# Kernel optimization log

Measured on AMD Instinct MI355X. Metric: run time of the kernel, lower is better.

Reference implementation:

```python
import jax, jax.numpy as jnp
import numpy as np

D_MODEL = 1024
N_HEAD = 16
HEAD_DIM = D_MODEL // N_HEAD
B, S = 4, 2048


def setup_inputs() -> dict:
    key = jax.random.key(0)
    ks = jax.random.split(key, 11)
    s = 1.0 / np.sqrt(D_MODEL)
    return {
        "query": jax.random.normal(ks[0], (B, S, D_MODEL), jnp.float32),
        "key": jax.random.normal(ks[1], (B, S, D_MODEL), jnp.float32),
        "value": jax.random.normal(ks[2], (B, S, D_MODEL), jnp.float32),
        "Wq": jax.random.normal(ks[3], (D_MODEL, D_MODEL), jnp.float32) * s,
        "bq": jax.random.normal(ks[4], (D_MODEL,), jnp.float32) * s,
        "Wk": jax.random.normal(ks[5], (D_MODEL, D_MODEL), jnp.float32) * s,
        "bk": jax.random.normal(ks[6], (D_MODEL,), jnp.float32) * s,
        "Wv": jax.random.normal(ks[7], (D_MODEL, D_MODEL), jnp.float32) * s,
        "bv": jax.random.normal(ks[8], (D_MODEL,), jnp.float32) * s,
        "Wo": jax.random.normal(ks[9], (D_MODEL, D_MODEL), jnp.float32) * s,
        "bo": jax.random.normal(ks[10], (D_MODEL,), jnp.float32) * s,
    }


def reference(query, key, value, Wq, bq, Wk, bk, Wv, bv, Wo, bo):
    b, s, d_model = query.shape
    # projections; reshape to [b, h, s, hd]
    def proj(x, W, bias):
        return (x @ W + bias).reshape(b, s, N_HEAD, HEAD_DIM).transpose(0, 2, 1, 3)
    q = proj(query, Wq, bq)
    k = proj(key, Wk, bk)
    v = proj(value, Wv, bv)
    # NOTE: original code scales by sqrt(d_model) (bug-faithful), not sqrt(head_dim)
    scores = jnp.einsum("bhqd,bhkd->bhqk", q, k) / jnp.sqrt(jnp.float32(d_model))
    causal = jnp.tril(jnp.ones((s, s), dtype=bool))
    scores = jnp.where(causal[None, None], scores, -jnp.inf)
    p = jax.nn.softmax(scores, axis=-1)  # dropout is identity in eval
    x = jnp.einsum("bhqk,bhkd->bhqd", p, v)
    x = x.transpose(0, 2, 1, 3).reshape(b, s, d_model)
    return x @ Wo + bo
```

## Files before the change

### kernel.cpp

```cpp
#include <hip/hip_runtime.h>
#include <hip/hip_bf16.h>
#include <cstdint>
#include <cstddef>

#define D_MODEL 1024
#define N_HEAD 16
#define HEAD_DIM 64
#define BATCH 4
#define SEQ 2048
#define M_ROWS (BATCH * SEQ)

typedef __attribute__((ext_vector_type(8))) short short8v;
typedef __attribute__((ext_vector_type(4))) float f32x4;
typedef __attribute__((ext_vector_type(16))) float f32x16;

__device__ __forceinline__ unsigned short f2bf(float f) {
    union { uint32_t i; float f; } c;
    c.f = f;
    uint32_t r = c.i + 0x7FFFu + ((c.i >> 16) & 1u);
    return (unsigned short)(r >> 16);
}
__device__ __forceinline__ unsigned short trunc_bf(float f) {
    return (unsigned short)(__float_as_uint(f) >> 16);
}
__device__ __forceinline__ uint32_t pack_trunc2(float a, float b) {
    return __builtin_amdgcn_perm(__float_as_uint(b), __float_as_uint(a), 0x07060302u);
}

struct __align__(16) U4 { uint32_t x, y, z, w; };
struct __align__(8) U2 { uint32_t x, y; };

__device__ __forceinline__ int sw_off(int row, int gl) {
    return row * 64 + ((gl ^ (row & 7)) << 3);
}

__global__ __launch_bounds__(256)
void wtrans_kernel(const float *__restrict__ W, unsigned short *__restrict__ Wt)
{
    __shared__ float tile[32][33];
    const int t = threadIdx.x;
    const int tx = t & 31, ty = t >> 5;
    const int bk = blockIdx.y * 32, bn = blockIdx.x * 32;
#pragma unroll
    for (int i = 0; i < 4; i++)
        tile[ty + 8 * i][tx] = W[(size_t)(bk + ty + 8 * i) * D_MODEL + bn + tx];
    __syncthreads();
#pragma unroll
    for (int i = 0; i < 4; i++)
        Wt[(size_t)(bn + ty + 8 * i) * D_MODEL + bk + tx] = trunc_bf(tile[tx][ty + 8 * i]);
}

template <typename TA, int MODE, typename TO>
__global__ __launch_bounds__(256, 2)
void mgemm_kernel(const TA *__restrict__ A,
                  const unsigned short *__restrict__ Wt,
                  const float *__restrict__ bias,
                  TO *__restrict__ out,
                  float escale)
{
    __shared__ __align__(16) unsigned short At[128 * 64];
    __shared__ __align__(16) unsigned short Bt[128 * 64];

    const int t = threadIdx.x;
    const int wave = t >> 6;
    const int lane = t & 63;
    const int n_ = lane & 15;
    const int quad = lane >> 4;
    const int wm = wave >> 1, wn = wave & 1;
    const int m0 = blockIdx.x * 128;
    const int n0 = blockIdx.y * 128;

    f32x4 acc[4][4];
#pragma unroll
    for (int i = 0; i < 4; i++)
#pragma unroll
        for (int j = 0; j < 4; j++) acc[i][j] = (f32x4){0.f, 0.f, 0.f, 0.f};

    const int srow = t >> 3;
    const int sg = t & 7;

    for (int k0 = 0; k0 < D_MODEL; k0 += 64) {
        __syncthreads();
#pragma unroll
        for (int i = 0; i < 4; i++) {
            const int r = srow + 32 * i;
            if constexpr (sizeof(TA) == 4) {
                const float *p = (const float *)A + (size_t)(m0 + r) * D_MODEL + k0 + sg * 8;
                float4 lo = *(const float4 *)p;
                float4 hi = *(const float4 *)(p + 4);
                U4 pk;
                pk.x = pack_trunc2(lo.x, lo.y);
                pk.y = pack_trunc2(lo.z, lo.w);
                pk.z = pack_trunc2(hi.x, hi.y);
                pk.w = pack_trunc2(hi.z, hi.w);
                *(U4 *)&At[sw_off(r, sg)] = pk;
            } else {
                const unsigned short *p =
                    (const unsigned short *)A + (size_t)(m0 + r) * D_MODEL + k0 + sg * 8;
                *(U4 *)&At[sw_off(r, sg)] = *(const U4 *)p;
            }
        }
#pragma unroll
        for (int i = 0; i < 4; i++) {
            const int r = srow + 32 * i;
            const unsigned short *p = Wt + (size_t)(n0 + r) * D_MODEL + k0 + sg * 8;
            *(U4 *)&Bt[sw_off(r, sg)] = *(const U4 *)p;
        }
        __syncthreads();

#pragma unroll
        for (int c = 0; c < 2; c++) {
            short8v af[4], bf[4];
#pragma unroll
            for (int mt = 0; mt < 4; mt++)
                af[mt] = *(const short8v *)&At[sw_off(wm * 64 + mt * 16 + n_, c * 4 + quad)];
#pragma unroll
            for (int nt = 0; nt < 4; nt++)
                bf[nt] = *(const short8v *)&Bt[sw_off(wn * 64 + nt * 16 + n_, c * 4 + quad)];
#pragma unroll
            for (int mt = 0; mt < 4; mt++)
#pragma unroll
                for (int nt = 0; nt < 4; nt++)
                    acc[mt][nt] =
                        __builtin_amdgcn_mfma_f32_16x16x32_bf16(af[mt], bf[nt], acc[mt][nt], 0, 0, 0);
        }
    }

    float bi[4];
#pragma unroll
    for (int nt = 0; nt < 4; nt++) bi[nt] = bias[n0 + wn * 64 + nt * 16 + n_];

#pragma unroll
    for (int mt = 0; mt < 4; mt++) {
#pragma unroll
        for (int reg = 0; reg < 4; reg++) {
            const int m = m0 + wm * 64 + mt * 16 + quad * 4 + reg;
#pragma unroll
            for (int nt = 0; nt < 4; nt++) {
                const int col = n0 + wn * 64 + nt * 16 + n_;
                const float v = (acc[mt][nt][reg] + bi[nt]) * escale;
                if constexpr (MODE == 1) {
                    ((unsigned short *)out)[(size_t)m * D_MODEL + col] = f2bf(v);
                } else if constexpr (MODE == 2) {
                    const size_t idx = ((size_t)(m >> 11) * D_MODEL + col) * SEQ + (m & 2047);
                    ((unsigned short *)out)[idx] = f2bf(v);
                } else {
                    ((float *)out)[(size_t)m * D_MODEL + col] = v;
                }
            }
        }
    }
}

__global__ __launch_bounds__(256, 2)
void attn_kernel(const unsigned short *Qg,
                 const unsigned short *__restrict__ Kg,
                 const unsigned short *__restrict__ VTg,
                 unsigned short *AO)
{
    __shared__ __align__(16) unsigned short Kt[64 * 64];
    __shared__ __align__(16) unsigned short Vt[64 * 64];

    const int h = blockIdx.x;
    const int b = blockIdx.y;
    const int qpair = blockIdx.z;
    const int t = threadIdx.x;
    const int w = t >> 6;
    const int lane = t & 63;
    const int ql = lane & 31;
    const int hi = lane >> 5;

    const size_t row_base = (size_t)b * SEQ * D_MODEL + h * HEAD_DIM;
    const size_t vhead = (size_t)(b * N_HEAD + h) * HEAD_DIM * SEQ;

    const int r0 = t >> 3;
    const int g = t & 7;

#pragma unroll
    for (int pass = 0; pass < 2; ++pass) {
        const int qb = pass ? (15 - qpair) : qpair;
        const int qs0 = qb * 128 + w * 32;
        const int qseq = qs0 + ql;

        short8v qf[4];
#pragma unroll
        for (int c = 0; c < 4; c++)
            qf[c] = *(const short8v *)(Qg + row_base + (size_t)qseq * D_MODEL + c * 16 + hi * 8);

        float m_i = -INFINITY, l_i = 0.f;
        f32x16 Oacc[2];
#pragma unroll
        for (int dt = 0; dt < 2; dt++)
#pragma unroll
            for (int i = 0; i < 16; i++) Oacc[dt][i] = 0.f;

        const int kb_max = 2 * qb + 1;

        for (int kb = 0; kb <= kb_max; ++kb) {
            __syncthreads();
#pragma unroll
            for (int i = 0; i < 2; i++) {
                const int r = r0 + 32 * i;
                U4 kv = *(const U4 *)(Kg + row_base + (size_t)(kb * 64 + r) * D_MODEL + g * 8);
                *(U4 *)&Kt[sw_off(r, g)] = kv;
                U4 vv = *(const U4 *)(VTg + vhead + (size_t)r * SEQ + kb * 64 + g * 8);
                *(U4 *)&Vt[sw_off(r, g)] = vv;
            }
            __syncthreads();

            if (kb * 64 > qs0 + 31) continue;

            f32x16 st[2];
            __builtin_amdgcn_s_setprio(1);
#pragma unroll
            for (int kt = 0; kt < 2; kt++) {
#pragma unroll
                for (int i = 0; i < 16; i++) st[kt][i] = 0.f;
#pragma unroll
                for (int c = 0; c < 4; c++) {
                    short8v kf = *(const short8v *)&Kt[sw_off(kt * 32 + ql, c * 2 + hi)];
                    st[kt] = __builtin_amdgcn_mfma_f32_32x32x16_bf16(kf, qf[c], st[kt], 0, 0, 0);
                }
            }
            __builtin_amdgcn_s_setprio(0);

            if (kb * 64 + 63 > qs0) {
#pragma unroll
                for (int kt = 0; kt < 2; kt++)
#pragma unroll
                    for (int r = 0; r < 16; r++) {
                        const int kseq = kb * 64 + kt * 32 + (r & 3) + 8 * (r >> 2) + 4 * hi;
                        if (kseq > qseq) st[kt][r] = -INFINITY;
                    }
            }

            float mx = -INFINITY;
#pragma unroll
            for (int kt = 0; kt < 2; kt++)
#pragma unroll
                for (int r = 0; r < 16; r++) mx = fmaxf(mx, st[kt][r]);
            mx = fmaxf(mx, __shfl_xor(mx, 32, 64));
            const float mnew = fmaxf(m_i, mx);
            const float alpha = __builtin_amdgcn_exp2f(m_i - mnew);
            m_i = mnew;
            float rs = 0.f;
#pragma unroll
            for (int kt = 0; kt < 2; kt++)
#pragma unroll
                for (int r = 0; r < 16; r++) {
                    const float p = __builtin_amdgcn_exp2f(st[kt][r] - mnew);
                    st[kt][r] = p;
                    rs += p;
                }
            rs += __shfl_xor(rs, 32, 64);
            l_i = l_i * alpha + rs;
#pragma unroll
            for (int dt = 0; dt < 2; dt++)
#pragma unroll
                for (int r = 0; r < 16; r++) Oacc[dt][r] *= alpha;

            short8v pf[4];
#pragma unroll
            for (int tt = 0; tt < 4; tt++) {
                const int kt = tt >> 1, o = (tt & 1) * 8;
                const uint32_t A  = pack_trunc2(st[kt][o + 0], st[kt][o + 1]);
                const uint32_t A2 = pack_trunc2(st[kt][o + 2], st[kt][o + 3]);
                const uint32_t B  = pack_trunc2(st[kt][o + 4], st[kt][o + 5]);
                const uint32_t B2 = pack_trunc2(st[kt][o + 6], st[kt][o + 7]);
                const uint32_t c1 = (uint32_t)__shfl_xor((int)(hi ? A : B), 32, 64);
                const uint32_t c2 = (uint32_t)__shfl_xor((int)(hi ? A2 : B2), 32, 64);
                union { uint32_t u[4]; short8v s; } cv;
                cv.u[0] = hi ? c1 : A;
                cv.u[1] = hi ? c2 : A2;
                cv.u[2] = hi ? B : c1;
                cv.u[3] = hi ? B2 : c2;
                pf[tt] = cv.s;
            }

            __builtin_amdgcn_s_setprio(1);
#pragma unroll
            for (int dt = 0; dt < 2; dt++)
#pragma unroll
                for (int tt = 0; tt < 4; tt++) {
                    short8v vf = *(const short8v *)&Vt[sw_off(dt * 32 + ql, tt * 2 + hi)];
                    Oacc[dt] = __builtin_amdgcn_mfma_f32_32x32x16_bf16(vf, pf[tt], Oacc[dt], 0, 0, 0);
                }
            __builtin_amdgcn_s_setprio(0);
        }

        const float linv = 1.f / l_i;
        const size_t obase = row_base + (size_t)qseq * D_MODEL;
#pragma unroll
        for (int dt = 0; dt < 2; dt++)
#pragma unroll
            for (int rg = 0; rg < 4; rg++) {
                const int d0 = dt * 32 + 8 * rg + 4 * hi;
                U2 pk;
                pk.x = (uint32_t)f2bf(Oacc[dt][4 * rg + 0] * linv) |
                       ((uint32_t)f2bf(Oacc[dt][4 * rg + 1] * linv) << 16);
                pk.y = (uint32_t)f2bf(Oacc[dt][4 * rg + 2] * linv) |
                       ((uint32_t)f2bf(Oacc[dt][4 * rg + 3] * linv) << 16);
                *(U2 *)(AO + obase + d0) = pk;
            }
    }
}

extern "C" void kernel_launch(void *const *d_in, const int *in_sizes, int n_in,
                              void *d_out, int out_size, void *d_ws, size_t ws_size,
                              hipStream_t stream)
{
    const float *q  = (const float *)d_in[0];
    const float *k  = (const float *)d_in[1];
    const float *v  = (const float *)d_in[2];
    const float *Wq = (const float *)d_in[3];
    const float *bq = (const float *)d_in[4];
    const float *Wk = (const float *)d_in[5];
    const float *bk = (const float *)d_in[6];
    const float *Wv = (const float *)d_in[7];
    const float *bv = (const float *)d_in[8];
    const float *Wo = (const float *)d_in[9];
    const float *bo = (const float *)d_in[10];
    float *out = (float *)d_out;

    const size_t TENS = (size_t)M_ROWS * D_MODEL;
    unsigned short *qbuf = (unsigned short *)d_ws;
    unsigned short *kbuf = qbuf + TENS;
    unsigned short *vtbuf = kbuf + TENS;
    unsigned short *wt = vtbuf + TENS;

    dim3 wgrid(32, 32);
    dim3 ggrid(M_ROWS / 128, D_MODEL / 128);

    const float qscale = 0.03125f * 1.44269504088896341f;

    wtrans_kernel<<<wgrid, 256, 0, stream>>>(Wq, wt);
    mgemm_kernel<float, 1, unsigned short><<<ggrid, 256, 0, stream>>>(q, wt, bq, qbuf, qscale);
    wtrans_kernel<<<wgrid, 256, 0, stream>>>(Wk, wt);
    mgemm_kernel<float, 1, unsigned short><<<ggrid, 256, 0, stream>>>(k, wt, bk, kbuf, 1.f);
    wtrans_kernel<<<wgrid, 256, 0, stream>>>(Wv, wt);
    mgemm_kernel<float, 2, unsigned short><<<ggrid, 256, 0, stream>>>(v, wt, bv, vtbuf, 1.f);

    attn_kernel<<<dim3(N_HEAD, BATCH, SEQ / 256), 256, 0, stream>>>(qbuf, kbuf, vtbuf, qbuf);

    wtrans_kernel<<<wgrid, 256, 0, stream>>>(Wo, wt);
    mgemm_kernel<unsigned short, 3, float><<<ggrid, 256, 0, stream>>>(qbuf, wt, bo, out, 1.f);
}
```

Baseline: 381.0 us.

## Use direct global-to-LDS loads for bf16 GEMM operands and pre-convert activations

New measurement: 323.0 us. 15.2% less time.

```diff
diff --git a/kernel.cpp b/kernel.cpp
--- a/kernel.cpp
+++ b/kernel.cpp
@@ -32,6 +32,25 @@
 
 __device__ __forceinline__ int sw_off(int row, int gl) {
     return row * 64 + ((gl ^ (row & 7)) << 3);
+}
+
+__device__ __forceinline__ void gload16(const unsigned short *g, unsigned short *l) {
+    __builtin_amdgcn_global_load_lds((const __attribute__((address_space(1))) void *)g,
+                                     (__attribute__((address_space(3))) void *)l, 16, 0, 0);
+}
+
+__global__ __launch_bounds__(256)
+void cvt_kernel(const float *__restrict__ src, unsigned short *__restrict__ dst)
+{
+    const size_t i = ((size_t)blockIdx.x * 256 + threadIdx.x) * 8;
+    float4 lo = *(const float4 *)(src + i);
+    float4 hi = *(const float4 *)(src + i + 4);
+    U4 pk;
+    pk.x = pack_trunc2(lo.x, lo.y);
+    pk.y = pack_trunc2(lo.z, lo.w);
+    pk.z = pack_trunc2(hi.x, hi.y);
+    pk.w = pack_trunc2(hi.z, hi.w);
+    *(U4 *)(dst + i) = pk;
 }
 
 __global__ __launch_bounds__(256)
@@ -78,13 +97,24 @@
 
     const int srow = t >> 3;
     const int sg = t & 7;
+    const int rl = lane >> 3;
+    const int gsw = (lane & 7) ^ rl;
 
     for (int k0 = 0; k0 < D_MODEL; k0 += 64) {
         __syncthreads();
-#pragma unroll
-        for (int i = 0; i < 4; i++) {
-            const int r = srow + 32 * i;
-            if constexpr (sizeof(TA) == 4) {
+        if constexpr (sizeof(TA) == 2) {
+#pragma unroll
+            for (int c = 0; c < 4; c++) {
+                const int rb = wave * 32 + c * 8;
+                gload16((const unsigned short *)A + (size_t)(m0 + rb + rl) * D_MODEL + k0 + (gsw << 3),
+                        &At[rb * 64]);
+                gload16(Wt + (size_t)(n0 + rb + rl) * D_MODEL + k0 + (gsw << 3),
+                        &Bt[rb * 64]);
+            }
+        } else {
+#pragma unroll
+            for (int i = 0; i < 4; i++) {
+                const int r = srow + 32 * i;
                 const float *p = (const float *)A + (size_t)(m0 + r) * D_MODEL + k0 + sg * 8;
                 float4 lo = *(const float4 *)p;
                 float4 hi = *(const float4 *)(p + 4);
@@ -94,17 +124,13 @@
                 pk.z = pack_trunc2(hi.x, hi.y);
                 pk.w = pack_trunc2(hi.z, hi.w);
                 *(U4 *)&At[sw_off(r, sg)] = pk;
-            } else {
-                const unsigned short *p =
-                    (const unsigned short *)A + (size_t)(m0 + r) * D_MODEL + k0 + sg * 8;
-                *(U4 *)&At[sw_off(r, sg)] = *(const U4 *)p;
-            }
-        }
-#pragma unroll
-        for (int i = 0; i < 4; i++) {
-            const int r = srow + 32 * i;
-            const unsigned short *p = Wt + (size_t)(n0 + r) * D_MODEL + k0 + sg * 8;
-            *(U4 *)&Bt[sw_off(r, sg)] = *(const U4 *)p;
+            }
+#pragma unroll
+            for (int i = 0; i < 4; i++) {
+                const int r = srow + 32 * i;
+                const unsigned short *p = Wt + (size_t)(n0 + r) * D_MODEL + k0 + sg * 8;
+                *(U4 *)&Bt[sw_off(r, sg)] = *(const U4 *)p;
+            }
         }
         __syncthreads();
 
@@ -326,22 +352,46 @@
     unsigned short *qbuf = (unsigned short *)d_ws;
     unsigned short *kbuf = qbuf + TENS;
     unsigned short *vtbuf = kbuf + TENS;
-    unsigned short *wt = vtbuf + TENS;
+    unsigned short *cbuf = vtbuf + TENS;
+    unsigned short *wt_new = cbuf + TENS;
+    unsigned short *wt_old = vtbuf + TENS;
 
     dim3 wgrid(32, 32);
     dim3 ggrid(M_ROWS / 128, D_MODEL / 128);
+    const int cgrid = (int)(TENS / 8 / 256);
 
     const float qscale = 0.03125f * 1.44269504088896341f;
 
-    wtrans_kernel<<<wgrid, 256, 0, stream>>>(Wq, wt);
-    mgemm_kernel<float, 1, unsigned short><<<ggrid, 256, 0, stream>>>(q, wt, bq, qbuf, qscale);
-    wtrans_kernel<<<wgrid, 256, 0, stream>>>(Wk, wt);
-    mgemm_kernel<float, 1, unsigned short><<<ggrid, 256, 0, stream>>>(k, wt, bk, kbuf, 1.f);
-    wtrans_kernel<<<wgrid, 256, 0, stream>>>(Wv, wt);
-    mgemm_kernel<float, 2, unsigned short><<<ggrid, 256, 0, stream>>>(v, wt, bv, vtbuf, 1.f);
-
-    attn_kernel<<<dim3(N_HEAD, BATCH, SEQ / 256), 256, 0, stream>>>(qbuf, kbuf, vtbuf, qbuf);
-
-    wtrans_kernel<<<wgrid, 256, 0, stream>>>(Wo, wt);
-    mgemm_kernel<unsigned short, 3, float><<<ggrid, 256, 0, stream>>>(qbuf, wt, bo, out, 1.f);
-}
+    const size_t need_new = (5 * TENS + (size_t)D_MODEL * D_MODEL) * sizeof(unsigned short);
+
+    if (ws_size >= need_new) {
+        unsigned short *wt = wt_new;
+        wtrans_kernel<<<wgrid, 256, 0, stream>>>(Wq, wt);
+        cvt_kernel<<<cgrid, 256, 0, stream>>>(q, cbuf);
+        mgemm_kernel<unsigned short, 1, unsigned short><<<ggrid, 256, 0, stream>>>(cbuf, wt, bq, qbuf, qscale);
+        wtrans_kernel<<<wgrid, 256, 0, stream>>>(Wk, wt);
+        cvt_kernel<<<cgrid, 256, 0, stream>>>(k, cbuf);
+        mgemm_kernel<unsigned short, 1, unsigned short><<<ggrid, 256, 0, stream>>>(cbuf, wt, bk, kbuf, 1.f);
+        wtrans_kernel<<<wgrid, 256, 0, stream>>>(Wv, wt);
+        cvt_kernel<<<cgrid, 256, 0, stream>>>(v, cbuf);
+        mgemm_kernel<unsigned short, 2, unsigned short><<<ggrid, 256, 0, stream>>>(cbuf, wt, bv, vtbuf, 1.f);
+
+        attn_kernel<<<dim3(N_HEAD, BATCH, SEQ / 256), 256, 0, stream>>>(qbuf, kbuf, vtbuf, qbuf);
+
+        wtrans_kernel<<<wgrid, 256, 0, stream>>>(Wo, wt);
+        mgemm_kernel<unsigned short, 3, float><<<ggrid, 256, 0, stream>>>(qbuf, wt, bo, out, 1.f);
+    } else {
+        unsigned short *wt = wt_old;
+        wtrans_kernel<<<wgrid, 256, 0, stream>>>(Wq, wt);
+        mgemm_kernel<float, 1, unsigned short><<<ggrid, 256, 0, stream>>>(q, wt, bq, qbuf, qscale);
+        wtrans_kernel<<<wgrid, 256, 0, stream>>>(Wk, wt);
+        mgemm_kernel<float, 1, unsigned short><<<ggrid, 256, 0, stream>>>(k, wt, bk, kbuf, 1.f);
+        wtrans_kernel<<<wgrid, 256, 0, stream>>>(Wv, wt);
+        mgemm_kernel<float, 2, unsigned short><<<ggrid, 256, 0, stream>>>(v, wt, bv, vtbuf, 1.f);
+
+        attn_kernel<<<dim3(N_HEAD, BATCH, SEQ / 256), 256, 0, stream>>>(qbuf, kbuf, vtbuf, qbuf);
+
+        wtrans_kernel<<<wgrid, 256, 0, stream>>>(Wo, wt);
+        mgemm_kernel<unsigned short, 3, float><<<ggrid, 256, 0, stream>>>(qbuf, wt, bo, out, 1.f);
+    }
+}
```
